# Optimization experiments

Hardware: AMD Instinct MI355X
Metric: run time of the kernel (lower is better)

## Reference

```python
import jax, jax.numpy as jnp
import numpy as np

WS = 8                       # window size (square)
N = WS * WS                  # tokens per window
RES_H, RES_W = 32, 32        # input_resolution
DIM = 512
NUM_HEADS = 16
HEAD_DIM = DIM // NUM_HEADS
SCALE = HEAD_DIM ** -0.5
TABLE = 2 * WS - 1           # size of a_p/b_p/a_r/b_r tables
B_ = 1024                    # num_windows * batch


def _rel_coords():
    c = np.arange(WS)
    coords = np.stack(np.meshgrid(c, c, indexing='ij'))          # (2, WS, WS)
    cf = coords.reshape(2, -1)                                   # (2, N)
    rel = cf[:, :, None] - cf[:, None, :]                        # (2, N, N), values in [-(WS-1), WS-1]
    return rel[0], rel[1]                                        # radius (dh), azimuth (dw)

RADIUS_NP, AZIMUTH_NP = _rel_coords()
# torch indexes the (2*WS-1)-row tables with negative indices -> python wrap: -k maps to TABLE-k
IDX_R = jnp.asarray(RADIUS_NP % TABLE)
IDX_AZ = jnp.asarray(AZIMUTH_NP % TABLE)
RADIUS = jnp.asarray(RADIUS_NP, dtype=jnp.float32)               # (N, N)
AZIMUTH = jnp.asarray(AZIMUTH_NP, dtype=jnp.float32)             # (N, N)


def setup_inputs() -> dict:
    key = jax.random.key(0)
    ks = jax.random.split(key, 10)
    return {
        'x': jax.random.normal(ks[0], (B_, N, DIM), dtype=jnp.float32),
        'theta_max': jnp.ones((), dtype=jnp.float32) * 1.5708,   # ~pi/2 field-of-view half-angle
        'qkv_w': jax.random.normal(ks[1], (3 * DIM, DIM), dtype=jnp.float32) * 0.02,
        'qkv_b': jnp.zeros((3 * DIM,), dtype=jnp.float32),
        'proj_w': jax.random.normal(ks[2], (DIM, DIM), dtype=jnp.float32) * 0.02,
        'proj_b': jnp.zeros((DIM,), dtype=jnp.float32),
        'a_p': jax.random.normal(ks[3], (TABLE, NUM_HEADS), dtype=jnp.float32) * 0.02,
        'b_p': jax.random.normal(ks[4], (TABLE, NUM_HEADS), dtype=jnp.float32) * 0.02,
        'a_r': jax.random.normal(ks[5], (TABLE, NUM_HEADS), dtype=jnp.float32) * 0.02,
        'b_r': jax.random.normal(ks[6], (TABLE, NUM_HEADS), dtype=jnp.float32) * 0.02,
    }


def _trig_bias(table_a, table_b, idx, angle):
    # table_[ab]: (TABLE, H); idx: (N, N) int; angle: (N, N) float (possibly traced)
    a = table_a[idx]                                              # (N, N, H)
    b = table_b[idx]
    ang = angle[:, :, None]                                       # (N, N, 1)
    bias = a * jnp.cos(ang) + b * jnp.sin(ang)                    # (N, N, H)
    return jnp.transpose(bias, (2, 0, 1))                         # (H, N, N)


def reference(x, theta_max, qkv_w, qkv_b, proj_w, proj_b, a_p, b_p, a_r, b_r):
    Bw, n, c = x.shape
    qkv = x @ qkv_w.T + qkv_b                                     # (B_, N, 3*DIM)
    qkv = qkv.reshape(Bw, n, 3, NUM_HEADS, HEAD_DIM)
    qkv = jnp.transpose(qkv, (2, 0, 3, 1, 4))                     # (3, B_, H, N, hd)
    q, k, v = qkv[0] * SCALE, qkv[1], qkv[2]

    attn = jnp.einsum('bhid,bhjd->bhij', q, k)                    # (B_, H, N, N)

    az_angle = AZIMUTH * (2.0 * np.pi / RES_W)                    # (N, N)
    A_phi = _trig_bias(a_p, b_p, IDX_AZ, az_angle)                # (H, N, N)
    r_angle = RADIUS * (theta_max / RES_H)                        # (N, N), traced via theta_max
    A_theta = _trig_bias(a_r, b_r, IDX_R, r_angle)                # (H, N, N)

    attn = attn + A_phi[None] + A_theta[None]
    attn = jax.nn.softmax(attn, axis=-1)

    out = jnp.einsum('bhij,bhjd->bhid', attn, v)                  # (B_, H, N, hd)
    out = jnp.transpose(out, (0, 2, 1, 3)).reshape(Bw, n, c)      # (B_, N, DIM)
    out = out @ proj_w.T + proj_b
    return out
```

## Files before the change

### kernel.cpp

```cpp
#include <hip/hip_runtime.h>
#include <hip/hip_bf16.h>


typedef __bf16 bf16_t;
typedef bf16_t bf16x4 __attribute__((ext_vector_type(4)));
typedef bf16_t bf16x8 __attribute__((ext_vector_type(8)));
typedef float  f32x4  __attribute__((ext_vector_type(4)));

#define NWIN   1024
#define NTOK   64
#define DIM    512
#define NHEADS 16
#define HD     32
#define MTOT   (NWIN*NTOK)
#define QKVN   (3*DIM)
#define SCLG2E 0.25503494f

__device__ __forceinline__ void async_copy16(const void* g, void* lds_generic) {
    __builtin_amdgcn_global_load_lds(
        (__attribute__((address_space(1))) unsigned int*)(unsigned long long)g,
        (__attribute__((address_space(3))) unsigned int*)(unsigned int)(unsigned long long)lds_generic,
        16, 0, 0);
}

__global__ void cvt_f32_bf16(const float* __restrict__ in, bf16_t* __restrict__ out, int n8) {
    int i = blockIdx.x * blockDim.x + threadIdx.x;
    if (i >= n8) return;
    const float4* p = (const float4*)in;
    float4 a = p[2*i], b = p[2*i+1];
    bf16x8 o;
    o[0]=(bf16_t)a.x; o[1]=(bf16_t)a.y; o[2]=(bf16_t)a.z; o[3]=(bf16_t)a.w;
    o[4]=(bf16_t)b.x; o[5]=(bf16_t)b.y; o[6]=(bf16_t)b.z; o[7]=(bf16_t)b.w;
    ((bf16x8*)out)[i] = o;
}

__global__ void bias_kernel(const float* __restrict__ ap, const float* __restrict__ bp,
                            const float* __restrict__ ar, const float* __restrict__ br,
                            const float* __restrict__ theta_max, float* __restrict__ bias) {
    int idx = blockIdx.x * 256 + threadIdx.x;
    int h  = idx >> 12;
    int ij = idx & 4095;
    int i = ij >> 6, j = ij & 63;
    int ri = i >> 3, ci = i & 7, rj = j >> 3, cj = j & 7;
    int rad = ri - rj, az = ci - cj;
    int idx_r  = rad < 0 ? rad + 15 : rad;
    int idx_az = az  < 0 ? az  + 15 : az;
    float azang = (float)az * 0.19634954084936207f;
    float rang  = (float)rad * (theta_max[0] * (1.0f/32.0f));
    float v = ap[idx_az*NHEADS + h] * cosf(azang) + bp[idx_az*NHEADS + h] * sinf(azang)
            + ar[idx_r *NHEADS + h] * cosf(rang)  + br[idx_r *NHEADS + h] * sinf(rang);
    bias[idx] = v * 1.4426950408889634f;
}

template<int OUT_BF16>
__global__ __launch_bounds__(256, 2)
void gemm_bt(const bf16_t* __restrict__ A, const bf16_t* __restrict__ Bt,
             const float* __restrict__ bias, void* __restrict__ C,
             int M, int N, int K, int ntiles) {
    __shared__ bf16_t sA[128*64];
    __shared__ bf16_t sB[128*64];

    int bid = blockIdx.x;
    int bm = bid / ntiles, bn = bid % ntiles;
    int tid = threadIdx.x;
    int w = tid >> 6, lane = tid & 63;
    int quad = lane >> 4, l16 = lane & 15;
    int wm = w >> 1, wn = w & 1;

    f32x4 acc[4][4] = {};

    const bf16_t* Abase = A  + (size_t)(bm*128) * K;
    const bf16_t* Bbase = Bt + (size_t)(bn*128) * K;

    for (int k0 = 0; k0 < K; k0 += 64) {
        for (int i = 0; i < 4; ++i) {
            int off = w*4096 + i*1024 + lane*16;
            int r  = off >> 7;
            int pb = (off >> 4) & 7;
            int cb = pb ^ (r & 7);
            async_copy16(Abase + (size_t)r*K + k0 + cb*8, (char*)sA + w*4096 + i*1024);
            async_copy16(Bbase + (size_t)r*K + k0 + cb*8, (char*)sB + w*4096 + i*1024);
        }
        __syncthreads();

        for (int kk = 0; kk < 64; kk += 32) {
            bf16x8 af[4], bf[4];
            for (int mi = 0; mi < 4; ++mi) {
                int r  = wm*64 + mi*16 + l16;
                int cb = (kk >> 3) + quad;
                int pb = cb ^ (r & 7);
                af[mi] = *(const bf16x8*)((const char*)sA + r*128 + pb*16);
            }
            for (int ni = 0; ni < 4; ++ni) {
                int r  = wn*64 + ni*16 + l16;
                int cb = (kk >> 3) + quad;
                int pb = cb ^ (r & 7);
                bf[ni] = *(const bf16x8*)((const char*)sB + r*128 + pb*16);
            }
            for (int mi = 0; mi < 4; ++mi)
                for (int ni = 0; ni < 4; ++ni)
                    acc[mi][ni] = __builtin_amdgcn_mfma_f32_16x16x32_bf16(
                        af[mi], bf[ni], acc[mi][ni], 0, 0, 0);
        }
        __syncthreads();
    }

    for (int ni = 0; ni < 4; ++ni) {
        int col = bn*128 + wn*64 + ni*16 + l16;
        float bv = bias[col];
        for (int mi = 0; mi < 4; ++mi) {
            int row0 = bm*128 + wm*64 + mi*16 + quad*4;
            f32x4 a = acc[mi][ni];
            for (int reg = 0; reg < 4; ++reg) {
                float v = a[reg] + bv;
                size_t o = (size_t)(row0 + reg) * N + col;
                if (OUT_BF16) ((bf16_t*)C)[o] = (bf16_t)v;
                else          ((float*)C)[o]  = v;
            }
        }
    }
}

__global__ __launch_bounds__(256, 4)
void attn_kernel(const bf16_t* __restrict__ qkv, const float* __restrict__ bias,
                 bf16_t* __restrict__ obuf) {
    __shared__ bf16_t pbuf[4][2048];

    int b = blockIdx.x;
    int tid = threadIdx.x;
    int w = tid >> 6, lane = tid & 63, quad = lane >> 4, l16 = lane & 15;
    int qh = quad >> 1, ql = quad & 1;
    const bf16_t* base = qkv + (size_t)(b*64) * QKVN;
    f32x4 zero = {0.f, 0.f, 0.f, 0.f};
    bf16_t* pb = pbuf[w];

    #pragma unroll 1
    for (int t = 0; t < 4; ++t) {
        int h = w*4 + t;

        bf16x8 ak[4], bq[4];
        #pragma unroll
        for (int jt = 0; jt < 4; ++jt)
            ak[jt] = *(const bf16x8*)(base + (size_t)(jt*16 + l16)*QKVN + 512 + h*32 + quad*8);
        #pragma unroll
        for (int it = 0; it < 4; ++it)
            bq[it] = *(const bf16x8*)(base + (size_t)(it*16 + l16)*QKVN + h*32 + quad*8);

        bf16x8 av[2][2];
        #pragma unroll
        for (int dt = 0; dt < 2; ++dt)
            #pragma unroll
            for (int ks = 0; ks < 2; ++ks) {
                const bf16_t* vb = base + (size_t)(ks*32 + quad*8)*QKVN + 1024 + h*32 + dt*16 + l16;
                bf16x8 tmp;
                #pragma unroll
                for (int e = 0; e < 8; ++e) tmp[e] = vb[(size_t)e*QKVN];
                av[dt][ks] = tmp;
            }

        const float* bh = bias + h*4096;
        f32x4 accO[2][4];
        float s[4];
        #pragma unroll
        for (int it = 0; it < 4; ++it) { s[it] = 0.f; accO[0][it] = zero; accO[1][it] = zero; }

        #pragma unroll
        for (int ks = 0; ks < 2; ++ks) {
            f32x4 bb[2][4];
            #pragma unroll
            for (int jh = 0; jh < 2; ++jh)
                #pragma unroll
                for (int it = 0; it < 4; ++it)
                    bb[jh][it] = *(const f32x4*)(bh + (it*16 + l16)*64 + (ks*2+jh)*16 + quad*4);

            f32x4 st[2][4];
            #pragma unroll
            for (int jh = 0; jh < 2; ++jh)
                #pragma unroll
                for (int it = 0; it < 4; ++it)
                    st[jh][it] = __builtin_amdgcn_mfma_f32_16x16x32_bf16(ak[ks*2+jh], bq[it], zero, 0, 0, 0);

            #pragma unroll
            for (int it = 0; it < 4; ++it)
                #pragma unroll
                for (int jh = 0; jh < 2; ++jh) {
                    float e0 = __builtin_amdgcn_exp2f(st[jh][it][0]*SCLG2E + bb[jh][it][0]);
                    float e1 = __builtin_amdgcn_exp2f(st[jh][it][1]*SCLG2E + bb[jh][it][1]);
                    float e2 = __builtin_amdgcn_exp2f(st[jh][it][2]*SCLG2E + bb[jh][it][2]);
                    float e3 = __builtin_amdgcn_exp2f(st[jh][it][3]*SCLG2E + bb[jh][it][3]);
                    s[it] += (e0 + e1) + (e2 + e3);
                    bf16x4 pk4;
                    pk4[0] = (bf16_t)e0; pk4[1] = (bf16_t)e1;
                    pk4[2] = (bf16_t)e2; pk4[3] = (bf16_t)e3;
                    *(bf16x4*)(pb + it*512 + (2*jh + qh)*128 + l16*8 + ql*4) = pk4;
                }

            #pragma unroll
            for (int it = 0; it < 4; ++it) {
                bf16x8 bp = ((const bf16x8*)(pb + it*512))[lane];
                accO[0][it] = __builtin_amdgcn_mfma_f32_16x16x32_bf16(av[0][ks], bp, accO[0][it], 0, 0, 0);
                accO[1][it] = __builtin_amdgcn_mfma_f32_16x16x32_bf16(av[1][ks], bp, accO[1][it], 0, 0, 0);
            }
        }

        #pragma unroll
        for (int it = 0; it < 4; ++it) {
            float sv = s[it];
            sv += __shfl_xor(sv, 16);
            sv += __shfl_xor(sv, 32);
            float inv = __builtin_amdgcn_rcpf(sv);
            #pragma unroll
            for (int dt = 0; dt < 2; ++dt) {
                bf16x4 o4;
                #pragma unroll
                for (int r = 0; r < 4; ++r) o4[r] = (bf16_t)(accO[dt][it][r] * inv);
                *(bf16x4*)(obuf + (size_t)(b*64 + it*16 + l16)*DIM + h*32 + dt*16 + quad*4) = o4;
            }
        }
    }
}

extern "C" void kernel_launch(void* const* d_in, const int* in_sizes, int n_in,
                              void* d_out, int out_size, void* d_ws, size_t ws_size,
                              hipStream_t stream) {
    const float* x      = (const float*)d_in[0];
    const float* theta  = (const float*)d_in[1];
    const float* qkv_w  = (const float*)d_in[2];
    const float* qkv_b  = (const float*)d_in[3];
    const float* proj_w = (const float*)d_in[4];
    const float* proj_b = (const float*)d_in[5];
    const float* a_p    = (const float*)d_in[6];
    const float* b_p    = (const float*)d_in[7];
    const float* a_r    = (const float*)d_in[8];
    const float* b_r    = (const float*)d_in[9];
    float* out = (float*)d_out;

    char* ws = (char*)d_ws;
    bf16_t* qkvbuf = (bf16_t*)ws;
    bf16_t* xb     = (bf16_t*)(ws + 201326592);
    bf16_t* wqkv   = (bf16_t*)(ws + 201326592 + 67108864);
    bf16_t* wproj  = (bf16_t*)(ws + 201326592 + 67108864 + 1572864);
    float*  biasbf = (float*) (ws + 201326592 + 67108864 + 1572864 + 524288);
    bf16_t* obuf   = xb;

    cvt_f32_bf16<<<(MTOT*DIM/8)/256, 256, 0, stream>>>(x, xb, MTOT*DIM/8);
    cvt_f32_bf16<<<(QKVN*DIM/8)/256, 256, 0, stream>>>(qkv_w, wqkv, QKVN*DIM/8);
    cvt_f32_bf16<<<(DIM*DIM/8)/256, 256, 0, stream>>>(proj_w, wproj, DIM*DIM/8);

    bias_kernel<<<256, 256, 0, stream>>>(a_p, b_p, a_r, b_r, theta, biasbf);

    gemm_bt<1><<<(MTOT/128)*(QKVN/128), 256, 0, stream>>>(xb, wqkv, qkv_b, qkvbuf,
                                                          MTOT, QKVN, DIM, QKVN/128);
    attn_kernel<<<NWIN, 256, 0, stream>>>(qkvbuf, biasbf, obuf);

    gemm_bt<0><<<(MTOT/128)*(DIM/128), 256, 0, stream>>>(obuf, wproj, proj_b, out,
                                                         MTOT, DIM, DIM, DIM/128);
}
```

Baseline: 535.2 us.

## Triple-buffer GEMM with async loads, 256x128 tiles, and XCD-aware block remap

Rewrites the bf16 GEMM to use 512-thread blocks over 256x128 output tiles with a three-stage LDS ring buffer. Global-to-LDS async copies for tile t+2 are issued while MFMAs run on tile t, gated by vmcnt waits and a single barrier per iteration. Block IDs are remapped with a stride of 8 so neighbouring tiles land on the same XCD for L2 reuse. This costs much more LDS (about 144KB per block) and more registers, which may limit occupancy to one block per CU.

```diff
diff --git a/kernel.cpp b/kernel.cpp
--- a/kernel.cpp
+++ b/kernel.cpp
@@ -53,64 +53,101 @@
 }
 
 template<int OUT_BF16>
-__global__ __launch_bounds__(256, 2)
+__global__ __launch_bounds__(512, 2)
 void gemm_bt(const bf16_t* __restrict__ A, const bf16_t* __restrict__ Bt,
              const float* __restrict__ bias, void* __restrict__ C,
              int M, int N, int K, int ntiles) {
-    __shared__ bf16_t sA[128*64];
-    __shared__ bf16_t sB[128*64];
-
+    __shared__ bf16_t sA[3][256*64];
+    __shared__ bf16_t sB[3][128*64];
+
+    int nwg = gridDim.x;
     int bid = blockIdx.x;
-    int bm = bid / ntiles, bn = bid % ntiles;
+    int wg = ((nwg & 7) == 0) ? ((bid & 7) * (nwg >> 3) + (bid >> 3)) : bid;
+    int bm = wg / ntiles, bn = wg % ntiles;
+
     int tid = threadIdx.x;
     int w = tid >> 6, lane = tid & 63;
     int quad = lane >> 4, l16 = lane & 15;
-    int wm = w >> 1, wn = w & 1;
-
-    f32x4 acc[4][4] = {};
-
-    const bf16_t* Abase = A  + (size_t)(bm*128) * K;
+    int wm = w >> 2, wn = w & 3;
+
+    const bf16_t* Abase = A  + (size_t)(bm*256) * K;
     const bf16_t* Bbase = Bt + (size_t)(bn*128) * K;
 
-    for (int k0 = 0; k0 < K; k0 += 64) {
+    int T = K >> 6;
+
+    auto STAGE = [&](int t) {
+        int q = t - (t/3)*3;
+        int k0 = t << 6;
+        #pragma unroll
         for (int i = 0; i < 4; ++i) {
-            int off = w*4096 + i*1024 + lane*16;
+            int off = (i*512 + tid) << 4;
             int r  = off >> 7;
             int pb = (off >> 4) & 7;
             int cb = pb ^ (r & 7);
-            async_copy16(Abase + (size_t)r*K + k0 + cb*8, (char*)sA + w*4096 + i*1024);
-            async_copy16(Bbase + (size_t)r*K + k0 + cb*8, (char*)sB + w*4096 + i*1024);
-        }
-        __syncthreads();
-
+            async_copy16(Abase + (size_t)r*K + k0 + cb*8,
+                         (char*)sA[q] + i*8192 + w*1024);
+        }
+        #pragma unroll
+        for (int i = 0; i < 2; ++i) {
+            int off = (i*512 + tid) << 4;
+            int r  = off >> 7;
+            int pb = (off >> 4) & 7;
+            int cb = pb ^ (r & 7);
+            async_copy16(Bbase + (size_t)r*K + k0 + cb*8,
+                         (char*)sB[q] + i*8192 + w*1024);
+        }
+    };
+
+    f32x4 acc[8][2] = {};
+
+    STAGE(0);
+    if (T > 1) STAGE(1);
+
+    #pragma unroll 1
+    for (int t = 0; t < T; ++t) {
+        if (t < T - 1) asm volatile("s_waitcnt vmcnt(6)" ::: "memory");
+        else           asm volatile("s_waitcnt vmcnt(0)" ::: "memory");
+        __builtin_amdgcn_s_barrier();
+        if (t + 2 < T) STAGE(t + 2);
+
+        int q = t - (t/3)*3;
+        const char* cA = (const char*)sA[q];
+        const char* cB = (const char*)sB[q];
+        #pragma unroll
         for (int kk = 0; kk < 64; kk += 32) {
-            bf16x8 af[4], bf[4];
-            for (int mi = 0; mi < 4; ++mi) {
-                int r  = wm*64 + mi*16 + l16;
+            bf16x8 af[8], bfr[2];
+            #pragma unroll
+            for (int mi = 0; mi < 8; ++mi) {
+                int r  = wm*128 + mi*16 + l16;
                 int cb = (kk >> 3) + quad;
                 int pb = cb ^ (r & 7);
-                af[mi] = *(const bf16x8*)((const char*)sA + r*128 + pb*16);
-            }
-            for (int ni = 0; ni < 4; ++ni) {
-                int r  = wn*64 + ni*16 + l16;
+                af[mi] = *(const bf16x8*)(cA + r*128 + pb*16);
+            }
+            #pragma unroll
+            for (int ni = 0; ni < 2; ++ni) {
+                int r  = wn*32 + ni*16 + l16;
                 int cb = (kk >> 3) + quad;
                 int pb = cb ^ (r & 7);
-                bf[ni] = *(const bf16x8*)((const char*)sB + r*128 + pb*16);
-            }
-            for (int mi = 0; mi < 4; ++mi)
-                for (int ni = 0; ni < 4; ++ni)
+                bfr[ni] = *(const bf16x8*)(cB + r*128 + pb*16);
+            }
+            #pragma unroll
+            for (int mi = 0; mi < 8; ++mi)
+                #pragma unroll
+                for (int ni = 0; ni < 2; ++ni)
                     acc[mi][ni] = __builtin_amdgcn_mfma_f32_16x16x32_bf16(
-                        af[mi], bf[ni], acc[mi][ni], 0, 0, 0);
-        }
-        __syncthreads();
+                        af[mi], bfr[ni], acc[mi][ni], 0, 0, 0);
+        }
     }
 
-    for (int ni = 0; ni < 4; ++ni) {
-        int col = bn*128 + wn*64 + ni*16 + l16;
+    #pragma unroll
+    for (int ni = 0; ni < 2; ++ni) {
+        int col = bn*128 + wn*32 + ni*16 + l16;
         float bv = bias[col];
-        for (int mi = 0; mi < 4; ++mi) {
-            int row0 = bm*128 + wm*64 + mi*16 + quad*4;
+        #pragma unroll
+        for (int mi = 0; mi < 8; ++mi) {
+            int row0 = bm*256 + wm*128 + mi*16 + quad*4;
             f32x4 a = acc[mi][ni];
+            #pragma unroll
             for (int reg = 0; reg < 4; ++reg) {
                 float v = a[reg] + bv;
                 size_t o = (size_t)(row0 + reg) * N + col;
@@ -249,10 +286,10 @@
 
     bias_kernel<<<256, 256, 0, stream>>>(a_p, b_p, a_r, b_r, theta, biasbf);
 
-    gemm_bt<1><<<(MTOT/128)*(QKVN/128), 256, 0, stream>>>(xb, wqkv, qkv_b, qkvbuf,
+    gemm_bt<1><<<(MTOT/256)*(QKVN/128), 512, 0, stream>>>(xb, wqkv, qkv_b, qkvbuf,
                                                           MTOT, QKVN, DIM, QKVN/128);
     attn_kernel<<<NWIN, 256, 0, stream>>>(qkvbuf, biasbf, obuf);
 
-    gemm_bt<0><<<(MTOT/128)*(DIM/128), 256, 0, stream>>>(obuf, wproj, proj_b, out,
+    gemm_bt<0><<<(MTOT/256)*(DIM/128), 512, 0, stream>>>(obuf, wproj, proj_b, out,
                                                          MTOT, DIM, DIM, DIM/128);
 }
```

After: 561.6 us. 4.9% more time.
